# Optimization experiments

Measured on AMD Instinct MI355X. Metric: run time of the kernel, lower is better.

## Reference

```python
import jax, jax.numpy as jnp
import numpy as np

D_HIDDEN = 512
N_HEADS = 8
D_HEAD = D_HIDDEN // N_HEADS
LAYER_IDX = 0
FACTOR = 0.5 / float(np.sqrt(D_HEAD))


def setup_inputs() -> dict:
    key = jax.random.key(0)
    ks = jax.random.split(key, 16)
    B, N, d = 4, 2048, D_HIDDEN
    s = 1.0 / float(np.sqrt(d))
    inp = {
        "H": jax.random.normal(ks[0], (B, N, d), jnp.float32),
        "V": jax.random.normal(ks[1], (B, N, 3, d), jnp.float32),
        "D": jax.random.normal(ks[2], (B, N, N), jnp.float32),
        "rbf": jax.random.normal(ks[3], (1, B, 1, N, N), jnp.float32),
        "mask": jnp.ones((B, N), jnp.int32),
        # learned parameters (torch nn.Linear: y = x @ W.T + b)
        "Wq": jax.random.normal(ks[4], (4 * d, d), jnp.float32) * s,
        "bq": jax.random.normal(ks[5], (4 * d,), jnp.float32) * s,
        "Wk": jax.random.normal(ks[6], (4 * d, d), jnp.float32) * s,
        "bk": jax.random.normal(ks[7], (4 * d,), jnp.float32) * s,
        "Wv": jax.random.normal(ks[8], (d, d), jnp.float32) * s,
        "bv": jax.random.normal(ks[9], (d,), jnp.float32) * s,
        "Wvv": jax.random.normal(ks[10], (d, d), jnp.float32) * s,
        "Wo": jax.random.normal(ks[11], (d, d), jnp.float32) * s,
        "bo": jax.random.normal(ks[12], (d,), jnp.float32) * s,
        "Wvo": jax.random.normal(ks[13], (d, d), jnp.float32) * s,
    }
    return inp


def reference(H, V, D, rbf, mask, Wq, bq, Wk, bk, Wv, bv, Wvv, Wo, bo, Wvo):
    B, N, d = H.shape
    nh, dh = N_HEADS, D_HEAD
    # projections
    Hq = (H @ Wq.T + bq).reshape(B, N, nh, 4 * dh)
    Hk = (H @ Wk.T + bk).reshape(B, N, nh, 4 * dh)
    Hv = (H @ Wv.T + bv).reshape(B, N, nh, dh)
    # vector values: [B,N,3,nh,dh] -> [B,N,nh,3,dh] -> [B,N,nh,3*dh]
    Vv = (V @ Wvv.T).reshape(B, N, 3, nh, dh)
    Vv = jnp.swapaxes(Vv, -2, -3).reshape(B, N, nh, 3 * dh)
    V_attn = jnp.concatenate([Hv, Vv], axis=-1)  # [B,N,nh,4*dh]
    # additive geometric bias + key mask
    bias = rbf[LAYER_IDX] + D[:, None]  # [B,1,N,N]
    bias = jnp.where(mask[:, None, None, :] == 0, -jnp.inf, bias)
    # attention
    scores = jnp.einsum('bnhd,bmhd->bhnm', Hq, Hk) * FACTOR + bias
    attn = jax.nn.softmax(scores, axis=-1)
    res = jnp.einsum('bhnm,bmhd->bnhd', attn, V_attn)  # [B,N,nh,4*dh]
    # split scalar / vector outputs
    H_res = res[..., :dh].reshape(B, N, d)
    V_res = res[..., dh:].reshape(B, N, nh, 3, dh)
    V_res = jnp.swapaxes(V_res, -2, -3).reshape(B, N, 3, d)
    H_o = H_res @ Wo.T + bo
    V_o = V_res @ Wvo.T
    return H_o, V_o
```

## Files before the change

kernel.cpp:

```cpp
#include <hip/hip_runtime.h>
#include <hip/hip_bf16.h>
#include <stdint.h>

typedef __hip_bfloat16 bf16;
typedef __attribute__((ext_vector_type(8))) short bf16x8;
typedef __attribute__((ext_vector_type(4))) float f32x4;
typedef __attribute__((ext_vector_type(16))) float f32x16;
typedef __attribute__((ext_vector_type(4))) unsigned short u16x4;

#define DEVI __device__ __forceinline__

static constexpr float FACTOR = 0.0625f;

DEVI unsigned short bfbits(float x) {
  return __builtin_bit_cast(unsigned short, __float2bfloat16(x));
}
DEVI float b2f(unsigned short u) {
  return __builtin_bit_cast(float, (uint32_t)u << 16);
}

__global__ void cvt_plain(const float* __restrict__ src, bf16* __restrict__ dst, int n) {
  int i = (blockIdx.x * 256 + threadIdx.x) * 4;
  if (i >= n) return;
  float4 v = *reinterpret_cast<const float4*>(src + i);
  union { unsigned short u[4]; uint64_t d; } t;
  t.u[0] = bfbits(v.x); t.u[1] = bfbits(v.y); t.u[2] = bfbits(v.z); t.u[3] = bfbits(v.w);
  *reinterpret_cast<uint64_t*>(dst + i) = t.d;
}

__global__ void cvt_vperm(const float* __restrict__ src, bf16* __restrict__ dst) {
  int g = blockIdx.x * 256 + threadIdx.x;
  int k4  = (g & 127) * 4;
  int rem = g >> 7;
  int c  = rem % 3;
  int bn = rem / 3;
  float4 v = *reinterpret_cast<const float4*>(src + (size_t)rem * 512 + k4);
  union { unsigned short u[4]; uint64_t d; } t;
  t.u[0] = bfbits(v.x); t.u[1] = bfbits(v.y); t.u[2] = bfbits(v.z); t.u[3] = bfbits(v.w);
  *reinterpret_cast<uint64_t*>(dst + ((size_t)c * 8192 + bn) * 512 + k4) = t.d;
}

__global__ void cvt_weights(const float* __restrict__ wq, const float* __restrict__ wk,
                            const float* __restrict__ wv, const float* __restrict__ wvv,
                            const float* __restrict__ wo, const float* __restrict__ wvo,
                            bf16* __restrict__ dst) {
  int blk = blockIdx.x;
  const float* s; int off;
  if      (blk < 1024) { s = wq  + blk * 1024;          off = 0       + blk * 1024; }
  else if (blk < 2048) { s = wk  + (blk - 1024) * 1024; off = 1048576 + (blk - 1024) * 1024; }
  else if (blk < 2304) { s = wv  + (blk - 2048) * 1024; off = 2097152 + (blk - 2048) * 1024; }
  else if (blk < 2560) { s = wvv + (blk - 2304) * 1024; off = 2359296 + (blk - 2304) * 1024; }
  else if (blk < 2816) { s = wo  + (blk - 2560) * 1024; off = 2621440 + (blk - 2560) * 1024; }
  else                 { s = wvo + (blk - 2816) * 1024; off = 2883584 + (blk - 2816) * 1024; }
  int i = threadIdx.x * 4;
  float4 v = *reinterpret_cast<const float4*>(s + i);
  union { unsigned short u[4]; uint64_t d; } t;
  t.u[0] = bfbits(v.x); t.u[1] = bfbits(v.y); t.u[2] = bfbits(v.z); t.u[3] = bfbits(v.w);
  *reinterpret_cast<uint64_t*>(dst + off + i) = t.d;
}

__global__ void bias_combine(const float* __restrict__ D, const float* __restrict__ rbf,
                             const int* __restrict__ mask, bf16* __restrict__ Bc) {
  size_t i = ((size_t)blockIdx.x * 256 + threadIdx.x) * 4;
  int col = (int)(i & 2047);
  int b   = (int)(i >> 22);
  float4 d = *reinterpret_cast<const float4*>(D + i);
  float4 r = *reinterpret_cast<const float4*>(rbf + i);
  const int* mrow = mask + b * 2048 + col;
  union { unsigned short u[4]; uint64_t dd; } t;
  t.u[0] = mrow[0] ? bfbits(d.x + r.x) : bfbits(-1e30f);
  t.u[1] = mrow[1] ? bfbits(d.y + r.y) : bfbits(-1e30f);
  t.u[2] = mrow[2] ? bfbits(d.z + r.z) : bfbits(-1e30f);
  t.u[3] = mrow[3] ? bfbits(d.w + r.w) : bfbits(-1e30f);
  *reinterpret_cast<uint64_t*>(Bc + i) = t.dd;
}

template<int MODE>
__global__ __launch_bounds__(256, 2) void gemm2(const bf16* __restrict__ A,
                                                const bf16* __restrict__ W,
                                                const bf16* __restrict__ W2,
                                                const float* __restrict__ bias,
                                                const float* __restrict__ bias2,
                                                void* __restrict__ outp) {
  constexpr int K = 512;
  __shared__ bf16 As[2][4096];
  __shared__ bf16 Bs[2][4096];
  const int tid = threadIdx.x;
  const int wid = tid >> 6, lane = tid & 63;
  const int lr = lane & 15, lg = lane >> 4;
  const int wr = wid >> 1, wc = wid & 1;
  const int bm = blockIdx.y * 128, bn = blockIdx.x * 128;

  const bf16* Wp;
  if constexpr (MODE == 0) Wp = W;
  else Wp = (blockIdx.y < 64) ? W : W2;

  const int q  = tid >> 2;
  const int ch = ((tid & 3) ^ ((tid >> 3) & 3)) * 8;
  const bf16* Asrc0 = A  + (size_t)(bm + q) * K + ch;
  const bf16* Asrc1 = A  + (size_t)(bm + 64 + q) * K + ch;
  const bf16* Wsrc0 = Wp + (size_t)(bn + q) * K + ch;
  const bf16* Wsrc1 = Wp + (size_t)(bn + 64 + q) * K + ch;
  const int wofs = wid * 1024;

  f32x4 acc[4][4];
#pragma unroll
  for (int m = 0; m < 4; m++)
#pragma unroll
    for (int n = 0; n < 4; n++) acc[m][n] = (f32x4){0.f, 0.f, 0.f, 0.f};

  __builtin_amdgcn_global_load_lds((const char*)Asrc0, (char*)&As[0][0] + wofs,        16, 0, 0);
  __builtin_amdgcn_global_load_lds((const char*)Asrc1, (char*)&As[0][0] + 4096 + wofs, 16, 0, 0);
  __builtin_amdgcn_global_load_lds((const char*)Wsrc0, (char*)&Bs[0][0] + wofs,        16, 0, 0);
  __builtin_amdgcn_global_load_lds((const char*)Wsrc1, (char*)&Bs[0][0] + 4096 + wofs, 16, 0, 0);
  __syncthreads();

  const int fxor = ((lr >> 1) & 3) << 4;
  for (int kt = 0; kt < 16; ++kt) {
    const int cur = kt & 1;
    if (kt < 15) {
      const int nxt = cur ^ 1;
      __builtin_amdgcn_global_load_lds((const char*)(Asrc0 + (kt + 1) * 32), (char*)&As[nxt][0] + wofs,        16, 0, 0);
      __builtin_amdgcn_global_load_lds((const char*)(Asrc1 + (kt + 1) * 32), (char*)&As[nxt][0] + 4096 + wofs, 16, 0, 0);
      __builtin_amdgcn_global_load_lds((const char*)(Wsrc0 + (kt + 1) * 32), (char*)&Bs[nxt][0] + wofs,        16, 0, 0);
      __builtin_amdgcn_global_load_lds((const char*)(Wsrc1 + (kt + 1) * 32), (char*)&Bs[nxt][0] + 4096 + wofs, 16, 0, 0);
    }
    const char* AsC = (const char*)&As[cur][0];
    const char* BsC = (const char*)&Bs[cur][0];
    bf16x8 af[4], bfr[4];
#pragma unroll
    for (int m = 0; m < 4; m++) {
      const int row = wr * 64 + m * 16 + lr;
      af[m] = *reinterpret_cast<const bf16x8*>(AsC + row * 64 + ((lg << 4) ^ fxor));
    }
#pragma unroll
    for (int n = 0; n < 4; n++) {
      const int row = wc * 64 + n * 16 + lr;
      bfr[n] = *reinterpret_cast<const bf16x8*>(BsC + row * 64 + ((lg << 4) ^ fxor));
    }
#pragma unroll
    for (int m = 0; m < 4; m++)
#pragma unroll
      for (int n = 0; n < 4; n++)
        acc[m][n] = __builtin_amdgcn_mfma_f32_16x16x32_bf16(af[m], bfr[n], acc[m][n], 0, 0, 0);
    __syncthreads();
  }

#pragma unroll
  for (int m = 0; m < 4; m++) {
#pragma unroll
    for (int n = 0; n < 4; n++) {
      const int col  = bn + wc * 64 + n * 16 + lr;
      const int row0 = bm + wr * 64 + m * 16 + lg * 4;
      if constexpr (MODE == 0) {
        const int isK = col >> 11;
        const int col2 = col & 2047;
        const float bb = isK ? bias2[col2] : bias[col2];
        const int hh = col2 >> 8, t = col2 & 255;
        bf16* out = (bf16*)outp + (size_t)isK * 16777216;
#pragma unroll
        for (int qq = 0; qq < 4; qq++) {
          const int row = row0 + qq;
          const int b = row >> 11, nn = row & 2047;
          float v = acc[m][n][qq] + bb;
          if (!isK) v *= FACTOR;
          out[(size_t)((b * 8 + hh) * 2048 + nn) * 256 + t] = __float2bfloat16(v);
        }
      } else if constexpr (MODE == 1) {
        bf16* out = (bf16*)outp;
        const int hh = col >> 6, t = col & 63;
        int dimrow, nn; float bb;
        if (row0 < 8192) {
          const int b = row0 >> 11; nn = row0 & 2047;
          dimrow = (b * 8 + hh) * 256 + t;
          bb = bias[col];
        } else {
          const int r = row0 - 8192;
          const int c = r >> 13, b = (r >> 11) & 3; nn = r & 2047;
          dimrow = (b * 8 + hh) * 256 + 64 + c * 64 + t;
          bb = 0.f;
        }
        const int i4 = (nn >> 2) & 7;
        const int o4 = (i4 & 4) | ((i4 & 1) << 1) | ((i4 >> 1) & 1);
        const int nn2 = (nn & ~31) | (o4 << 2);
        union { unsigned short u[4]; uint64_t d; } pk;
#pragma unroll
        for (int qq = 0; qq < 4; qq++) pk.u[qq] = bfbits(acc[m][n][qq] + bb);
        *reinterpret_cast<uint64_t*>(out + (size_t)dimrow * 2048 + nn2) = pk.d;
      } else {
        float* out = (float*)outp;
        if (row0 < 8192) {
          const float bb = bias[col];
#pragma unroll
          for (int qq = 0; qq < 4; qq++)
            out[(size_t)(row0 + qq) * 512 + col] = acc[m][n][qq] + bb;
        } else {
#pragma unroll
          for (int qq = 0; qq < 4; qq++)
            out[4194304 + (size_t)(row0 - 8192 + qq) * 512 + col] = acc[m][n][qq];
        }
      }
    }
  }
}

__global__ __launch_bounds__(256, 2) void attn_kernel(
    const bf16* __restrict__ Qg, const bf16* __restrict__ Kg, const bf16* __restrict__ Vtg,
    const bf16* __restrict__ Bc, bf16* __restrict__ Hres, bf16* __restrict__ Vres) {
  __shared__ bf16 Ks[2][32 * 256];
  __shared__ bf16 Vs[2][256 * 32];

  const int g = blockIdx.x;
  const int x = g & 7, loc = g >> 3;
  const int bh = x * 4 + (loc & 3);
  const int qt = loc >> 2;
  const int b = bh >> 3, h = bh & 7;
  const int tid = threadIdx.x, w = tid >> 6, lane = tid & 63;
  const int lq = lane & 31, hi = lane >> 5;
  const int q0 = qt * 128 + w * 32;

  const bf16* Qb = Qg + (size_t)bh * 2048 * 256;
  const char* KbC = (const char*)(Kg + (size_t)bh * 2048 * 256);
  const char* VbC = (const char*)(Vtg + (size_t)bh * 256 * 2048);
  const bf16* Bb = Bc + ((size_t)(b * 2048 + q0 + lq)) * 2048 + hi * 4;

  bf16x8 qf[16];
#pragma unroll
  for (int kc = 0; kc < 16; kc++)
    qf[kc] = *reinterpret_cast<const bf16x8*>(Qb + (size_t)(q0 + lq) * 256 + kc * 16 + hi * 8);

  f32x16 O[8];
#pragma unroll
  for (int dt = 0; dt < 8; dt++)
#pragma unroll
    for (int r = 0; r < 16; r++) O[dt][r] = 0.f;
  float mrun = -INFINITY, lrun = 0.f;

  const char* ksrc[4]; const char* vsrc[4];
#pragma unroll
  for (int i = 0; i < 4; i++) {
    const int krow = w * 8 + 2 * i + hi;
    ksrc[i] = KbC + (size_t)krow * 512 + ((lq * 16) ^ ((krow & 31) << 4));
    const int vrow = w * 64 + i * 16 + (lane >> 2);
    const int gg = ((vrow >> 1) ^ (vrow >> 3)) & 3;
    vsrc[i] = VbC + (size_t)vrow * 4096 + (((lane & 3) ^ gg) << 4);
  }

  {
    char* dK = (char*)&Ks[0][0] + w * 4096;
    char* dV = (char*)&Vs[0][0] + w * 4096;
#pragma unroll
    for (int i = 0; i < 4; i++) {
      __builtin_amdgcn_global_load_lds(ksrc[i], dK + i * 1024, 16, 0, 0);
      __builtin_amdgcn_global_load_lds(vsrc[i], dV + i * 1024, 16, 0, 0);
    }
  }
  asm volatile("s_waitcnt vmcnt(0)" ::: "memory");
  __builtin_amdgcn_sched_barrier(0);
  __builtin_amdgcn_s_barrier();

  for (int kt = 0; kt < 64; ++kt) {
    const int cur = kt & 1;
    u16x4 bg[4];
#pragma unroll
    for (int i = 0; i < 4; i++)
      bg[i] = *reinterpret_cast<const u16x4*>(Bb + kt * 32 + i * 8);
    if (kt < 63) {
      char* dK = (char*)&Ks[cur ^ 1][0] + w * 4096;
      char* dV = (char*)&Vs[cur ^ 1][0] + w * 4096;
#pragma unroll
      for (int i = 0; i < 4; i++) {
        __builtin_amdgcn_global_load_lds(ksrc[i] + (size_t)(kt + 1) * 16384, dK + i * 1024, 16, 0, 0);
        __builtin_amdgcn_global_load_lds(vsrc[i] + (size_t)(kt + 1) * 64,    dV + i * 1024, 16, 0, 0);
      }
    }
    __builtin_amdgcn_sched_barrier(0);

    const char* KsC = (const char*)&Ks[cur][0];
    f32x16 se, so;
#pragma unroll
    for (int r = 0; r < 16; r++) { se[r] = 0.f; so[r] = 0.f; }
    const int kxor = lq << 4;
#pragma unroll
    for (int kc = 0; kc < 16; kc += 2) {
      bf16x8 k0 = *reinterpret_cast<const bf16x8*>(KsC + lq * 512 + ((kc * 32 + hi * 16) ^ kxor));
      bf16x8 k1 = *reinterpret_cast<const bf16x8*>(KsC + lq * 512 + (((kc + 1) * 32 + hi * 16) ^ kxor));
      se = __builtin_amdgcn_mfma_f32_32x32x16_bf16(k0, qf[kc], se, 0, 0, 0);
      so = __builtin_amdgcn_mfma_f32_32x32x16_bf16(k1, qf[kc + 1], so, 0, 0, 0);
    }
    f32x16 s;
#pragma unroll
    for (int r = 0; r < 16; r++)
      s[r] = se[r] + so[r] + b2f((unsigned short)bg[r >> 2][r & 3]);

    float m0 = fmaxf(s[0], s[1]),  m1 = fmaxf(s[2], s[3]);
    float m2 = fmaxf(s[4], s[5]),  m3 = fmaxf(s[6], s[7]);
    float m4 = fmaxf(s[8], s[9]),  m5 = fmaxf(s[10], s[11]);
    float m6 = fmaxf(s[12], s[13]), m7 = fmaxf(s[14], s[15]);
    float pmax = fmaxf(fmaxf(fmaxf(m0, m1), fmaxf(m2, m3)),
                       fmaxf(fmaxf(m4, m5), fmaxf(m6, m7)));
    pmax = fmaxf(pmax, __shfl_xor(pmax, 32));

    const float mnew = fmaxf(mrun, pmax);
    const float scq = __expf(mrun - mnew);
    mrun = mnew;
    lrun *= scq;
    float sfac[16];
#pragma unroll
    for (int r = 0; r < 16; r++) sfac[r] = __shfl(scq, (r & 3) + 8 * (r >> 2) + 4 * hi);
#pragma unroll
    for (int dt = 0; dt < 8; dt++)
#pragma unroll
      for (int r = 0; r < 16; r++) O[dt][r] *= sfac[r];

    union { unsigned short u[8]; bf16x8 v; } pa0, pa1;
    float rs = 0.f;
#pragma unroll
    for (int j = 0; j < 8; j++) {
      const float p = __expf(s[j] - mrun);
      pa0.u[j] = bfbits(p);
      rs += b2f(pa0.u[j]);
    }
#pragma unroll
    for (int j = 0; j < 8; j++) {
      const float p = __expf(s[8 + j] - mrun);
      pa1.u[j] = bfbits(p);
      rs += b2f(pa1.u[j]);
    }
    rs += __shfl_xor(rs, 32);
    lrun += rs;

    const char* VsC = (const char*)&Vs[cur][0];
#pragma unroll
    for (int dt = 0; dt < 8; dt++) {
      const int row = dt * 32 + lq;
      const int gg = ((row >> 1) ^ (row >> 3)) & 3;
      bf16x8 v0 = *reinterpret_cast<const bf16x8*>(VsC + row * 64 + ((hi ^ gg) << 4));
      bf16x8 v1 = *reinterpret_cast<const bf16x8*>(VsC + row * 64 + (((2 + hi) ^ gg) << 4));
      O[dt] = __builtin_amdgcn_mfma_f32_32x32x16_bf16(pa0.v, v0, O[dt], 0, 0, 0);
      O[dt] = __builtin_amdgcn_mfma_f32_32x32x16_bf16(pa1.v, v1, O[dt], 0, 0, 0);
    }

    if (kt < 63) {
      asm volatile("s_waitcnt vmcnt(0)" ::: "memory");
      __builtin_amdgcn_sched_barrier(0);
      __builtin_amdgcn_s_barrier();
    }
  }

  const float rli = 1.0f / lrun;
  float rl[16];
#pragma unroll
  for (int r = 0; r < 16; r++) rl[r] = __shfl(rli, (r & 3) + 8 * (r >> 2) + 4 * hi);
#pragma unroll
  for (int dt = 0; dt < 8; dt++) {
    const int d = dt * 32 + lq;
#pragma unroll
    for (int r = 0; r < 16; r++) {
      const int row = q0 + (r & 3) + 8 * (r >> 2) + 4 * hi;
      const float v = O[dt][r] * rl[r];
      if (d < 64) {
        Hres[(size_t)(b * 2048 + row) * 512 + h * 64 + d] = __float2bfloat16(v);
      } else {
        const int c = (d - 64) >> 6, t = (d - 64) & 63;
        Vres[((size_t)(b * 2048 + row) * 3 + c) * 512 + h * 64 + t] = __float2bfloat16(v);
      }
    }
  }
}

extern "C" void kernel_launch(void* const* d_in, const int* in_sizes, int n_in,
                              void* d_out, int out_size, void* d_ws, size_t ws_size,
                              hipStream_t stream) {
  const float* H   = (const float*)d_in[0];
  const float* V   = (const float*)d_in[1];
  const float* Dm  = (const float*)d_in[2];
  const float* rbf = (const float*)d_in[3];
  const int*   mask= (const int*)d_in[4];
  const float* Wq  = (const float*)d_in[5];
  const float* bq  = (const float*)d_in[6];
  const float* Wk  = (const float*)d_in[7];
  const float* bk  = (const float*)d_in[8];
  const float* Wv  = (const float*)d_in[9];
  const float* bv  = (const float*)d_in[10];
  const float* Wvv = (const float*)d_in[11];
  const float* Wo  = (const float*)d_in[12];
  const float* bo  = (const float*)d_in[13];
  const float* Wvo = (const float*)d_in[14];

  char* ws = (char*)d_ws;
  bf16* Hbf  = (bf16*)(ws);
  bf16* Wall = (bf16*)(ws + 33554432);
  bf16* Qw   = (bf16*)(ws + 39845888);
  bf16* Kw   = Qw + 16777216;
  bf16* Vtw  = (bf16*)(ws + 106954752);
  bf16* Hres = Hbf;
  bf16* Wqb  = Wall;
  bf16* Wvb  = Wall + 2097152;
  bf16* Wvvb = Wall + 2359296;
  bf16* Wob  = Wall + 2621440;
  bf16* Wvob = Wall + 2883584;
  bf16* Bcb  = (bf16*)d_out;

  bias_combine<<<16384, 256, 0, stream>>>(Dm, rbf, mask, Bcb);
  cvt_plain<<<4096, 256, 0, stream>>>(H, Hbf, 4194304);
  cvt_vperm<<<12288, 256, 0, stream>>>(V, Hbf + 4194304);
  cvt_weights<<<3072, 256, 0, stream>>>(Wq, Wk, Wv, Wvv, Wo, Wvo, Wall);

  gemm2<0><<<dim3(32, 64), 256, 0, stream>>>(Hbf, Wqb, nullptr, bq, bk, Qw);
  gemm2<1><<<dim3(4, 256), 256, 0, stream>>>(Hbf, Wvb, Wvvb, bv, nullptr, Vtw);

  attn_kernel<<<512, 256, 0, stream>>>(Qw, Kw, Vtw, Bcb, Hres, Hbf + 4194304);

  gemm2<2><<<dim3(4, 256), 256, 0, stream>>>(Hbf, Wob, Wvob, bo, nullptr, d_out);
}
```

Measured before the change: 459.6 us.

## Use exp2 softmax with folded log2e, lazy rescale, single MFMA accumulator

Folds log2(e) into the Q scale and the precomputed bias so the attention softmax can use exp2f directly instead of __expf. Adds a lazy online-softmax rescale: the 8x16 output accumulator is rescaled only when some lane's block max exceeds the running max by more than 8 (in log2 units). Merges the two interleaved QK MFMA accumulator chains into one. This cuts per-tile exp and multiply work, but the single accumulator chain serializes MFMA dependencies, and the skipped rescale lets unnormalized values grow up to 2^8 before correction.

```diff
diff --git a/kernel.cpp b/kernel.cpp
--- a/kernel.cpp
+++ b/kernel.cpp
@@ -10,7 +10,8 @@
 
 #define DEVI __device__ __forceinline__
 
-static constexpr float FACTOR = 0.0625f;
+static constexpr float LOG2E = 1.44269504088896f;
+static constexpr float FACTOR_L2E = 0.0625f * 1.44269504088896f;
 
 DEVI unsigned short bfbits(float x) {
   return __builtin_bit_cast(unsigned short, __float2bfloat16(x));
@@ -68,10 +69,10 @@
   float4 r = *reinterpret_cast<const float4*>(rbf + i);
   const int* mrow = mask + b * 2048 + col;
   union { unsigned short u[4]; uint64_t dd; } t;
-  t.u[0] = mrow[0] ? bfbits(d.x + r.x) : bfbits(-1e30f);
-  t.u[1] = mrow[1] ? bfbits(d.y + r.y) : bfbits(-1e30f);
-  t.u[2] = mrow[2] ? bfbits(d.z + r.z) : bfbits(-1e30f);
-  t.u[3] = mrow[3] ? bfbits(d.w + r.w) : bfbits(-1e30f);
+  t.u[0] = mrow[0] ? bfbits((d.x + r.x) * LOG2E) : bfbits(-1e30f);
+  t.u[1] = mrow[1] ? bfbits((d.y + r.y) * LOG2E) : bfbits(-1e30f);
+  t.u[2] = mrow[2] ? bfbits((d.z + r.z) * LOG2E) : bfbits(-1e30f);
+  t.u[3] = mrow[3] ? bfbits((d.w + r.w) * LOG2E) : bfbits(-1e30f);
   *reinterpret_cast<uint64_t*>(Bc + i) = t.dd;
 }
 
@@ -163,7 +164,7 @@
           const int row = row0 + qq;
           const int b = row >> 11, nn = row & 2047;
           float v = acc[m][n][qq] + bb;
-          if (!isK) v *= FACTOR;
+          if (!isK) v *= FACTOR_L2E;
           out[(size_t)((b * 8 + hh) * 2048 + nn) * 256 + t] = __float2bfloat16(v);
         }
       } else if constexpr (MODE == 1) {
@@ -277,21 +278,18 @@
     __builtin_amdgcn_sched_barrier(0);
 
     const char* KsC = (const char*)&Ks[cur][0];
-    f32x16 se, so;
-#pragma unroll
-    for (int r = 0; r < 16; r++) { se[r] = 0.f; so[r] = 0.f; }
+    f32x16 s;
+#pragma unroll
+    for (int r = 0; r < 16; r++) s[r] = 0.f;
     const int kxor = lq << 4;
 #pragma unroll
-    for (int kc = 0; kc < 16; kc += 2) {
-      bf16x8 k0 = *reinterpret_cast<const bf16x8*>(KsC + lq * 512 + ((kc * 32 + hi * 16) ^ kxor));
-      bf16x8 k1 = *reinterpret_cast<const bf16x8*>(KsC + lq * 512 + (((kc + 1) * 32 + hi * 16) ^ kxor));
-      se = __builtin_amdgcn_mfma_f32_32x32x16_bf16(k0, qf[kc], se, 0, 0, 0);
-      so = __builtin_amdgcn_mfma_f32_32x32x16_bf16(k1, qf[kc + 1], so, 0, 0, 0);
-    }
-    f32x16 s;
+    for (int kc = 0; kc < 16; kc++) {
+      bf16x8 kf = *reinterpret_cast<const bf16x8*>(KsC + lq * 512 + ((kc * 32 + hi * 16) ^ kxor));
+      s = __builtin_amdgcn_mfma_f32_32x32x16_bf16(kf, qf[kc], s, 0, 0, 0);
+    }
 #pragma unroll
     for (int r = 0; r < 16; r++)
-      s[r] = se[r] + so[r] + b2f((unsigned short)bg[r >> 2][r & 3]);
+      s[r] += b2f((unsigned short)bg[r >> 2][r & 3]);
 
     float m0 = fmaxf(s[0], s[1]),  m1 = fmaxf(s[2], s[3]);
     float m2 = fmaxf(s[4], s[5]),  m3 = fmaxf(s[6], s[7]);
@@ -301,29 +299,32 @@
                        fmaxf(fmaxf(m4, m5), fmaxf(m6, m7)));
     pmax = fmaxf(pmax, __shfl_xor(pmax, 32));
 
-    const float mnew = fmaxf(mrun, pmax);
-    const float scq = __expf(mrun - mnew);
-    mrun = mnew;
-    lrun *= scq;
-    float sfac[16];
-#pragma unroll
-    for (int r = 0; r < 16; r++) sfac[r] = __shfl(scq, (r & 3) + 8 * (r >> 2) + 4 * hi);
-#pragma unroll
-    for (int dt = 0; dt < 8; dt++)
-#pragma unroll
-      for (int r = 0; r < 16; r++) O[dt][r] *= sfac[r];
+    const bool ok = (pmax <= mrun + 8.f);
+    if (!__all((int)ok)) {
+      const float mnew = fmaxf(mrun, pmax);
+      const float scq = exp2f(mrun - mnew);
+      mrun = mnew;
+      lrun *= scq;
+      float sfac[16];
+#pragma unroll
+      for (int r = 0; r < 16; r++) sfac[r] = __shfl(scq, (r & 3) + 8 * (r >> 2) + 4 * hi);
+#pragma unroll
+      for (int dt = 0; dt < 8; dt++)
+#pragma unroll
+        for (int r = 0; r < 16; r++) O[dt][r] *= sfac[r];
+    }
 
     union { unsigned short u[8]; bf16x8 v; } pa0, pa1;
     float rs = 0.f;
 #pragma unroll
     for (int j = 0; j < 8; j++) {
-      const float p = __expf(s[j] - mrun);
+      const float p = exp2f(s[j] - mrun);
       pa0.u[j] = bfbits(p);
       rs += b2f(pa0.u[j]);
     }
 #pragma unroll
     for (int j = 0; j < 8; j++) {
-      const float p = __expf(s[8 + j] - mrun);
+      const float p = exp2f(s[8 + j] - mrun);
       pa1.u[j] = bfbits(p);
       rs += b2f(pa1.u[j]);
     }
```

After: 441.8 us. -3.9%, faster.
